# Performance work log

Hardware: AMD Instinct MI355X
Metric: run time of the kernel (lower is better)

## Reference

```python
import jax, jax.numpy as jnp
import numpy as np

BATCH, TOP_K, MAX_LEN, EMB_DIM = 8, 64, 256, 768


def setup_inputs() -> dict:
    key = jax.random.key(0)
    context = jax.random.normal(key, (BATCH, TOP_K, 2, MAX_LEN, EMB_DIM), dtype=jnp.float32)
    return {"context": context}


def reference(context):
    # context: [B, K, 2, L, D]; slice 0 = context tokens, slice 1 = entity tokens
    ctx = context[:, :, 0, :, :]   # [B, K, L, D]
    ent = context[:, :, 1, :, :]   # [B, K, L, D]
    # similarity: for each context token, score against every entity token
    sim = jnp.einsum("bkld,bkmd->bklm", ctx, ent)  # [B, K, L, L]
    idx = jnp.argmax(sim, axis=-1)                 # [B, K, L] hard attention index
    # gather best-matching entity token per context token
    sel = jnp.take_along_axis(ent, idx[..., None], axis=2)  # [B, K, L, D]
    # dot product per token then sum over tokens (sum-of-max score)
    out = jnp.sum(ctx * sel, axis=(-1, -2))        # [B, K]
    return out
```

## Files before the change

kernel.cpp:

```cpp
#include <hip/hip_runtime.h>


#define MAXLEN 256
#define EMB 768
#define BK 64
#define NSTEP 12
#define LSTRIDE 72

typedef __attribute__((ext_vector_type(4))) float f32x4;
typedef __attribute__((ext_vector_type(8))) short short8;
typedef __bf16 bf16x8 __attribute__((ext_vector_type(8)));
typedef __bf16 bf16x4 __attribute__((ext_vector_type(4)));

__device__ inline bf16x8 cvt8(float4 a, float4 b) {
  bf16x8 r;
  r[0] = (__bf16)a.x; r[1] = (__bf16)a.y; r[2] = (__bf16)a.z; r[3] = (__bf16)a.w;
  r[4] = (__bf16)b.x; r[5] = (__bf16)b.y; r[6] = (__bf16)b.z; r[7] = (__bf16)b.w;
  return r;
}

__device__ inline uint2 cvt4u(float4 v) {
  union { uint2 u; bf16x4 h; } r;
  r.h[0] = (__bf16)v.x; r.h[1] = (__bf16)v.y;
  r.h[2] = (__bf16)v.z; r.h[3] = (__bf16)v.w;
  return r.u;
}

__global__ __launch_bounds__(1024, 4) void som_rowmax_kernel(
    const float* __restrict__ ctx_all, float* __restrict__ out) {
  __shared__ __align__(16) short lsB[2][MAXLEN][LSTRIDE];
  __shared__ float red[16];

  const int t    = threadIdx.x;
  const int w    = t >> 6;
  const int lane = t & 63;
  const int qw   = lane >> 4;
  const int lr   = lane & 15;

  const size_t p = blockIdx.x;
  const float* ctx = ctx_all + p * (size_t)(2 * MAXLEN * EMB);
  const float* ent = ctx + (size_t)(MAXLEN * EMB);

  const int srow = t >> 4;
  const int scol = (t & 15) * 4;
  const float* gB = ent + (size_t)srow * EMB + scol;

  const float* gA = ctx + (size_t)(16 * w + lr) * EMB + qw * 8;

  f32x4 acc[16];
  float4 rb[4];
  float4 ra0[2];
  float4 ra1[2];
  bf16x8 afr[2];

  auto issueB = [&](int s) {
#pragma unroll
    for (int j = 0; j < 4; ++j)
      rb[j] = *(const float4*)(gB + (size_t)j * (64 * EMB) + s * BK);
  };
  auto commitB = [&](int buf) {
#pragma unroll
    for (int j = 0; j < 4; ++j)
      *(uint2*)&lsB[buf][j * 64 + srow][scol] = cvt4u(rb[j]);
  };
  auto issueA0 = [&](int s) {
    ra0[0] = *(const float4*)(gA + s * BK + 0);
    ra0[1] = *(const float4*)(gA + s * BK + 4);
  };
  auto issueA1 = [&](int s) {
    ra1[0] = *(const float4*)(gA + s * BK + 32);
    ra1[1] = *(const float4*)(gA + s * BK + 36);
  };
  auto packA0 = [&]() { afr[0] = cvt8(ra0[0], ra0[1]); };
  auto packA1 = [&]() { afr[1] = cvt8(ra1[0], ra1[1]); };
  auto mfmaHalf = [&](int buf, int kh) {
    const int kq = kh * 32 + qw * 8;
#pragma unroll
    for (int mt = 0; mt < 16; ++mt) {
      bf16x8 bfr = __builtin_bit_cast(bf16x8, *(const short8*)&lsB[buf][mt * 16 + lr][kq]);
      acc[mt] = __builtin_amdgcn_mfma_f32_16x16x32_bf16(afr[kh], bfr, acc[mt], 0, 0, 0);
    }
  };
  auto barrier = [&]() {
    asm volatile("s_waitcnt lgkmcnt(0)" ::: "memory");
    __builtin_amdgcn_sched_barrier(0);
    __builtin_amdgcn_s_barrier();
    __builtin_amdgcn_sched_barrier(0);
  };

  issueB(0);
  issueA0(0);
  issueA1(0);
  commitB(0);
  issueB(1);
#pragma unroll
  for (int mt = 0; mt < 16; ++mt) acc[mt] = (f32x4){0.f, 0.f, 0.f, 0.f};
  packA0();
  packA1();
  barrier();

  for (int s = 0; s < NSTEP - 1; ++s) {
    issueA0(s + 1);
    issueA1(s + 1);
    commitB((s + 1) & 1);
    if (s + 2 < NSTEP) issueB(s + 2);
    mfmaHalf(s & 1, 0);
    mfmaHalf(s & 1, 1);
    packA0();
    packA1();
    barrier();
  }
  mfmaHalf((NSTEP - 1) & 1, 0);
  mfmaHalf((NSTEP - 1) & 1, 1);

  float s = 0.f;
#pragma unroll
  for (int i = 0; i < 4; ++i) {
    float m = acc[0][i];
#pragma unroll
    for (int mt = 1; mt < 16; ++mt) m = fmaxf(m, acc[mt][i]);
#pragma unroll
    for (int d = 1; d < 16; d <<= 1) m = fmaxf(m, __shfl_xor(m, d, 64));
    s += m;
  }
  s += __shfl_xor(s, 16, 64);
  s += __shfl_xor(s, 32, 64);

  if (lane == 0) red[w] = s;
  __syncthreads();
  if (t == 0) {
    float tot = 0.f;
#pragma unroll
    for (int i = 0; i < 16; ++i) tot += red[i];
    out[p] = tot;
  }
}

extern "C" void kernel_launch(void* const* d_in, const int* in_sizes, int n_in,
                              void* d_out, int out_size, void* d_ws, size_t ws_size,
                              hipStream_t stream) {
  const float* ctx_all = (const float*)d_in[0];
  float* out = (float*)d_out;
  som_rowmax_kernel<<<dim3(512), dim3(1024), 0, stream>>>(ctx_all, out);
}
```

Baseline: 153.4 us.

## Halve block to 512 threads, two row tiles per wave, deeper B prefetch

Blocks shrink from 1024 to 512 threads. Each wave now computes two 16-row tiles of context tokens, so every LDS fragment of entity tokens feeds two MFMAs, which halves LDS reads per MFMA. Global loads of B use two alternating register sets to prefetch two steps ahead. The cost is more VGPRs per thread (32 accumulators plus 16 float4 prefetch registers), which may reduce occupancy, and half as many waves are available to hide latency.

```diff
diff --git a/kernel.cpp b/kernel.cpp
--- a/kernel.cpp
+++ b/kernel.cpp
@@ -26,10 +26,10 @@
   return r.u;
 }
 
-__global__ __launch_bounds__(1024, 4) void som_rowmax_kernel(
+__global__ __launch_bounds__(512, 2) void som_rowmax_kernel(
     const float* __restrict__ ctx_all, float* __restrict__ out) {
   __shared__ __align__(16) short lsB[2][MAXLEN][LSTRIDE];
-  __shared__ float red[16];
+  __shared__ float red[8];
 
   const int t    = threadIdx.x;
   const int w    = t >> 6;
@@ -45,40 +45,50 @@
   const int scol = (t & 15) * 4;
   const float* gB = ent + (size_t)srow * EMB + scol;
 
-  const float* gA = ctx + (size_t)(16 * w + lr) * EMB + qw * 8;
+  const float* gA0 = ctx + (size_t)(32 * w + lr) * EMB + qw * 8;
+  const float* gA1 = ctx + (size_t)(32 * w + 16 + lr) * EMB + qw * 8;
 
-  f32x4 acc[16];
-  float4 rb[4];
-  float4 ra0[2];
-  float4 ra1[2];
-  bf16x8 afr[2];
+  f32x4 acc[2][16];
+  float4 rb0[8], rb1[8];
+  float4 ra[4];
+  bf16x8 afr[2][2];
 
-  auto issueB = [&](int s) {
+  auto issueB = [&](float4 (&rbc)[8], int s) {
 #pragma unroll
-    for (int j = 0; j < 4; ++j)
-      rb[j] = *(const float4*)(gB + (size_t)j * (64 * EMB) + s * BK);
+    for (int j = 0; j < 8; ++j)
+      rbc[j] = *(const float4*)(gB + (size_t)j * (32 * EMB) + s * BK);
   };
-  auto commitB = [&](int buf) {
+  auto commitB = [&](float4 (&rbc)[8], int buf) {
 #pragma unroll
-    for (int j = 0; j < 4; ++j)
-      *(uint2*)&lsB[buf][j * 64 + srow][scol] = cvt4u(rb[j]);
+    for (int j = 0; j < 8; ++j)
+      *(uint2*)&lsB[buf][j * 32 + srow][scol] = cvt4u(rbc[j]);
   };
-  auto issueA0 = [&](int s) {
-    ra0[0] = *(const float4*)(gA + s * BK + 0);
-    ra0[1] = *(const float4*)(gA + s * BK + 4);
+  auto issueA = [&](int s) {
+    ra[0] = *(const float4*)(gA0 + s * BK + 0);
+    ra[1] = *(const float4*)(gA0 + s * BK + 4);
+    ra[2] = *(const float4*)(gA1 + s * BK + 0);
+    ra[3] = *(const float4*)(gA1 + s * BK + 4);
   };
   auto issueA1 = [&](int s) {
-    ra1[0] = *(const float4*)(gA + s * BK + 32);
-    ra1[1] = *(const float4*)(gA + s * BK + 36);
+    ra[0] = *(const float4*)(gA0 + s * BK + 32);
+    ra[1] = *(const float4*)(gA0 + s * BK + 36);
+    ra[2] = *(const float4*)(gA1 + s * BK + 32);
+    ra[3] = *(const float4*)(gA1 + s * BK + 36);
   };
-  auto packA0 = [&]() { afr[0] = cvt8(ra0[0], ra0[1]); };
-  auto packA1 = [&]() { afr[1] = cvt8(ra1[0], ra1[1]); };
-  auto mfmaHalf = [&](int buf, int kh) {
-    const int kq = kh * 32 + qw * 8;
+  auto packA = [&](int kh) {
+    afr[0][kh] = cvt8(ra[0], ra[1]);
+    afr[1][kh] = cvt8(ra[2], ra[3]);
+  };
+  auto mfmaStep = [&](int buf) {
 #pragma unroll
-    for (int mt = 0; mt < 16; ++mt) {
-      bf16x8 bfr = __builtin_bit_cast(bf16x8, *(const short8*)&lsB[buf][mt * 16 + lr][kq]);
-      acc[mt] = __builtin_amdgcn_mfma_f32_16x16x32_bf16(afr[kh], bfr, acc[mt], 0, 0, 0);
+    for (int kh = 0; kh < 2; ++kh) {
+      const int kq = kh * 32 + qw * 8;
+#pragma unroll
+      for (int mt = 0; mt < 16; ++mt) {
+        bf16x8 bfr = __builtin_bit_cast(bf16x8, *(const short8*)&lsB[buf][mt * 16 + lr][kq]);
+        acc[0][mt] = __builtin_amdgcn_mfma_f32_16x16x32_bf16(afr[0][kh], bfr, acc[0][mt], 0, 0, 0);
+        acc[1][mt] = __builtin_amdgcn_mfma_f32_16x16x32_bf16(afr[1][kh], bfr, acc[1][mt], 0, 0, 0);
+      }
     }
   };
   auto barrier = [&]() {
@@ -88,40 +98,51 @@
     __builtin_amdgcn_sched_barrier(0);
   };
 
-  issueB(0);
-  issueA0(0);
+  auto body = [&](int s, float4 (&rbc)[8], bool issueNext) {
+    issueA(s + 1);
+    commitB(rbc, (s + 1) & 1);
+    if (issueNext) issueB(rbc, s + 3);
+    mfmaStep(s & 1);
+    packA(0);
+    issueA1(s + 1);
+    packA(1);
+    barrier();
+  };
+
+  issueB(rb0, 0);
+  issueA(0);
+  commitB(rb0, 0);
+  issueB(rb0, 1);
+#pragma unroll
+  for (int ti = 0; ti < 2; ++ti)
+#pragma unroll
+    for (int mt = 0; mt < 16; ++mt) acc[ti][mt] = (f32x4){0.f, 0.f, 0.f, 0.f};
+  packA(0);
   issueA1(0);
-  commitB(0);
-  issueB(1);
-#pragma unroll
-  for (int mt = 0; mt < 16; ++mt) acc[mt] = (f32x4){0.f, 0.f, 0.f, 0.f};
-  packA0();
-  packA1();
+  packA(1);
+  issueB(rb1, 2);
   barrier();
 
-  for (int s = 0; s < NSTEP - 1; ++s) {
-    issueA0(s + 1);
-    issueA1(s + 1);
-    commitB((s + 1) & 1);
-    if (s + 2 < NSTEP) issueB(s + 2);
-    mfmaHalf(s & 1, 0);
-    mfmaHalf(s & 1, 1);
-    packA0();
-    packA1();
-    barrier();
+#pragma unroll 1
+  for (int ss = 0; ss < 5; ++ss) {
+    body(2 * ss + 0, rb0, 2 * ss + 0 < 9);
+    body(2 * ss + 1, rb1, 2 * ss + 1 < 9);
   }
-  mfmaHalf((NSTEP - 1) & 1, 0);
-  mfmaHalf((NSTEP - 1) & 1, 1);
+  body(10, rb0, false);
+  mfmaStep(1);
 
   float s = 0.f;
 #pragma unroll
-  for (int i = 0; i < 4; ++i) {
-    float m = acc[0][i];
+  for (int ti = 0; ti < 2; ++ti) {
 #pragma unroll
-    for (int mt = 1; mt < 16; ++mt) m = fmaxf(m, acc[mt][i]);
+    for (int i = 0; i < 4; ++i) {
+      float m = acc[ti][0][i];
 #pragma unroll
-    for (int d = 1; d < 16; d <<= 1) m = fmaxf(m, __shfl_xor(m, d, 64));
-    s += m;
+      for (int mt = 1; mt < 16; ++mt) m = fmaxf(m, acc[ti][mt][i]);
+#pragma unroll
+      for (int d = 1; d < 16; d <<= 1) m = fmaxf(m, __shfl_xor(m, d, 64));
+      s += m;
+    }
   }
   s += __shfl_xor(s, 16, 64);
   s += __shfl_xor(s, 32, 64);
@@ -131,7 +152,7 @@
   if (t == 0) {
     float tot = 0.f;
 #pragma unroll
-    for (int i = 0; i < 16; ++i) tot += red[i];
+    for (int i = 0; i < 8; ++i) tot += red[i];
     out[p] = tot;
   }
 }
@@ -141,5 +162,5 @@
                               hipStream_t stream) {
   const float* ctx_all = (const float*)d_in[0];
   float* out = (float*)d_out;
-  som_rowmax_kernel<<<dim3(512), dim3(1024), 0, stream>>>(ctx_all, out);
+  som_rowmax_kernel<<<dim3(512), dim3(512), 0, stream>>>(ctx_all, out);
 }
```

Result: slower. 280.6 us (+82.9%).
